# Optimization experiments

Measured on AMD Instinct MI355X. Metric: run time of the kernel, lower is better.

## Reference

```python
import jax, jax.numpy as jnp
import numpy as np

N_NODES = 50000
N_EDGES = 800000
N_GRAPHS = 128
NEG_SLOPE = 0.2


def setup_inputs() -> dict:
    key = jax.random.key(0)
    ks = jax.random.split(key, 16)
    feature = jax.random.normal(ks[0], (N_NODES, 10), dtype=jnp.float32)
    src = jax.random.randint(ks[1], (N_EDGES,), 0, N_NODES, dtype=jnp.int32)
    dst = jax.random.randint(ks[2], (N_EDGES,), 0, N_NODES, dtype=jnp.int32)
    graph_ids = jnp.sort(jax.random.randint(ks[3], (N_NODES,), 0, N_GRAPHS, dtype=jnp.int32))
    s = 0.1
    W1 = jax.random.normal(ks[4], (10, 3 * 32), dtype=jnp.float32) * s
    al1 = jax.random.normal(ks[5], (3, 32), dtype=jnp.float32) * s
    ar1 = jax.random.normal(ks[6], (3, 32), dtype=jnp.float32) * s
    W2 = jax.random.normal(ks[7], (96, 3 * 64), dtype=jnp.float32) * s
    al2 = jax.random.normal(ks[8], (3, 64), dtype=jnp.float32) * s
    ar2 = jax.random.normal(ks[9], (3, 64), dtype=jnp.float32) * s
    d1_w = jax.random.normal(ks[10], (192, 64), dtype=jnp.float32) * s
    d1_b = jnp.zeros((64,), dtype=jnp.float32)
    d2_w = jax.random.normal(ks[11], (64, 1), dtype=jnp.float32) * s
    d2_b = jnp.zeros((1,), dtype=jnp.float32)
    return {"feature": feature, "src": src, "dst": dst, "graph_ids": graph_ids,
            "W1": W1, "al1": al1, "ar1": ar1, "W2": W2, "al2": al2, "ar2": ar2,
            "d1_w": d1_w, "d1_b": d1_b, "d2_w": d2_w, "d2_b": d2_b}


def _edge_softmax(e, dst, n_nodes):
    # e: [E, H] unnormalized logits; softmax over incoming edges of each dst node
    m = jax.ops.segment_max(e, dst, num_segments=n_nodes)  # [N, H]
    ex = jnp.exp(e - m[dst])
    s = jax.ops.segment_sum(ex, dst, num_segments=n_nodes)  # [N, H]
    return ex / (s[dst] + 1e-16)


def _gat_layer(x, W, al, ar, src, dst, n_nodes):
    H, D = al.shape
    z = (x @ W).reshape(n_nodes, H, D)                     # [N, H, D]
    el = jnp.einsum('nhd,hd->nh', z, al)                   # [N, H]
    er = jnp.einsum('nhd,hd->nh', z, ar)
    e = jax.nn.leaky_relu(el[src] + er[dst], NEG_SLOPE)    # [E, H]
    a = _edge_softmax(e, dst, n_nodes)                     # [E, H]
    msg = z[src] * a[:, :, None]                           # [E, H, D]
    out = jax.ops.segment_sum(msg, dst, num_segments=n_nodes)
    return out.reshape(n_nodes, H * D)


def reference(feature, src, dst, graph_ids, W1, al1, ar1, W2, al2, ar2, d1_w, d1_b, d2_w, d2_b):
    n = feature.shape[0]
    x1 = jax.nn.relu(_gat_layer(feature, W1, al1, ar1, src, dst, n))  # [N, 96]
    x2 = jax.nn.relu(_gat_layer(x1, W2, al2, ar2, src, dst, n))       # [N, 192]
    # AvgPooling: mean of node features per graph
    sums = jax.ops.segment_sum(x2, graph_ids, num_segments=N_GRAPHS)  # [G, 192]
    cnts = jax.ops.segment_sum(jnp.ones((n,), x2.dtype), graph_ids, num_segments=N_GRAPHS)
    pooled = sums / jnp.maximum(cnts, 1.0)[:, None]
    h = jax.nn.relu(pooled @ d1_w + d1_b)
    return h @ d2_w + d2_b  # [G, 1]
```

## Files before the change

kernel.cpp:

```cpp
#include <hip/hip_runtime.h>
#include <hip/hip_bf16.h>

#define NEG_SLOPE 0.2f

typedef __attribute__((ext_vector_type(8))) short short8v;
typedef __attribute__((ext_vector_type(4))) float f32x4;

__device__ __forceinline__ float wave_max64(float v) {
    for (int o = 32; o; o >>= 1) v = fmaxf(v, __shfl_xor(v, o));
    return v;
}
__device__ __forceinline__ float wave_sum64(float v) {
    for (int o = 32; o; o >>= 1) v += __shfl_xor(v, o);
    return v;
}
__device__ __forceinline__ unsigned short f2bf(float f) {
    unsigned int u = __float_as_uint(f);
    unsigned int r = (u + 0x7fffu + ((u >> 16) & 1u)) >> 16;
    return (unsigned short)r;
}
__device__ __forceinline__ float bf2f(unsigned short u) {
    return __uint_as_float(((unsigned int)u) << 16);
}
__device__ __forceinline__ float bflo(unsigned int pk) {
    return __uint_as_float(pk << 16);
}
__device__ __forceinline__ float bfhi(unsigned int pk) {
    return __uint_as_float(pk & 0xFFFF0000u);
}


__global__ __launch_bounds__(256) void k_hist(const int* __restrict__ dst,
                                              int* __restrict__ deg,
                                              int* __restrict__ rank, int E,
                                              const float* __restrict__ W2,
                                              const float* __restrict__ al2,
                                              const float* __restrict__ ar2,
                                              unsigned short* __restrict__ W2T,
                                              float* __restrict__ val2,
                                              float* __restrict__ var2) {
    int idx = blockIdx.x * 256 + threadIdx.x;
    if (idx < 96 * 192) {
        int c = idx / 96, k = idx - c * 96;
        W2T[idx] = f2bf(W2[k * 192 + c]);
    } else if (idx < 96 * 192 + 2 * 288) {
        int t = idx - 96 * 192;
        int which = t / 288;
        int tt = t - which * 288;
        int h = tt / 96, j = tt - h * 96;
        const float* av = which ? ar2 : al2;
        float a = 0.f;
        for (int d = 0; d < 64; d++) a += W2[j * 192 + h * 64 + d] * av[h * 64 + d];
        (which ? var2 : val2)[tt] = a;
    }
    if (idx < E) rank[idx] = atomicAdd(&deg[dst[idx]], 1);
}


__global__ __launch_bounds__(256) void k_scan1(const int* __restrict__ deg,
                                               int* __restrict__ bsum, int n) {
    int idx = blockIdx.x * 256 + threadIdx.x;
    int v = idx < n ? deg[idx] : 0;
    for (int o = 32; o; o >>= 1) v += __shfl_xor(v, o);
    __shared__ int ws[4];
    if ((threadIdx.x & 63) == 0) ws[threadIdx.x >> 6] = v;
    __syncthreads();
    if (threadIdx.x == 0) bsum[blockIdx.x] = ws[0] + ws[1] + ws[2] + ws[3];
}

__global__ __launch_bounds__(256) void k_scan2(const int* __restrict__ bsum,
                                               int* __restrict__ bpre,
                                               int* __restrict__ row_start,
                                               int nb, int n) {
    __shared__ int s[256];
    int t = threadIdx.x;
    int v = t < nb ? bsum[t] : 0;
    s[t] = v;
    __syncthreads();
    for (int o = 1; o < 256; o <<= 1) {
        int u = (t >= o) ? s[t - o] : 0;
        __syncthreads();
        s[t] += u;
        __syncthreads();
    }
    if (t < nb) bpre[t] = s[t] - v;
    if (t == 255) row_start[n] = s[255];
}

__global__ __launch_bounds__(256) void k_scan3(const int* __restrict__ deg,
                                               const int* __restrict__ bpre,
                                               int* __restrict__ row_start, int n) {
    int idx = blockIdx.x * 256 + threadIdx.x;
    int lane = threadIdx.x & 63;
    int w = threadIdx.x >> 6;
    int d = idx < n ? deg[idx] : 0;
    int x = d;
    for (int o = 1; o < 64; o <<= 1) {
        int u = __shfl_up(x, o);
        if (lane >= o) x += u;
    }
    __shared__ int ws[4];
    if (lane == 63) ws[w] = x;
    __syncthreads();
    int add = bpre[blockIdx.x];
    for (int i = 0; i < w; i++) add += ws[i];
    if (idx < n) row_start[idx] = add + x - d;
}

__global__ void k_scatter(const int* __restrict__ dst, const int* __restrict__ src,
                          const int* __restrict__ rank, const int* __restrict__ row_start,
                          int* __restrict__ ssrc, int E) {
    int e = blockIdx.x * blockDim.x + threadIdx.x;
    if (e < E) ssrc[row_start[dst[e]] + rank[e]] = src[e];
}


__global__ __launch_bounds__(256) void k_el1(const float* __restrict__ feat,
                                             const float* __restrict__ W1,
                                             const float* __restrict__ al,
                                             const float* __restrict__ ar,
                                             float4* __restrict__ el1,
                                             float4* __restrict__ er1, int n) {
    __shared__ float sW[960], sal[96], sar[96], sval[30], svar[30];
    for (int i = threadIdx.x; i < 960; i += 256) sW[i] = W1[i];
    for (int i = threadIdx.x; i < 96; i += 256) { sal[i] = al[i]; sar[i] = ar[i]; }
    __syncthreads();
    int t = threadIdx.x;
    if (t < 30) {
        int h = t / 10, k = t - h * 10;
        float a = 0.f, b = 0.f;
        for (int d = 0; d < 32; d++) {
            float wv = sW[k * 96 + h * 32 + d];
            a += wv * sal[h * 32 + d];
            b += wv * sar[h * 32 + d];
        }
        sval[t] = a; svar[t] = b;
    }
    __syncthreads();
    int nd = blockIdx.x * 256 + t;
    if (nd >= n) return;
    float x[10];
#pragma unroll
    for (int k = 0; k < 10; k++) x[k] = feat[(size_t)nd * 10 + k];
    float el[3] = {}, er[3] = {};
#pragma unroll
    for (int h = 0; h < 3; h++)
#pragma unroll
        for (int k = 0; k < 10; k++) {
            el[h] += x[k] * sval[h * 10 + k];
            er[h] += x[k] * svar[h * 10 + k];
        }
    el1[nd] = make_float4(el[0], el[1], el[2], 0.f);
    er1[nd] = make_float4(er[0], er[1], er[2], 0.f);
}


__global__ __launch_bounds__(256) void k_agg1(const float* __restrict__ feat,
                                              const float4* __restrict__ el,
                                              const float4* __restrict__ er,
                                              const int* __restrict__ row_start,
                                              const int* __restrict__ ssrc,
                                              float* __restrict__ y1, int n) {
    __shared__ float pl[4][272];
    int wid = (blockIdx.x * blockDim.x + threadIdx.x) >> 6;
    int lane = threadIdx.x & 63;
    int w = threadIdx.x >> 6;
    if (wid >= n) return;
    int s0 = row_start[wid];
    int deg = row_start[wid + 1] - s0;
    if (deg <= 0) {
        if (lane < 30) y1[(size_t)wid * 30 + lane] = 0.f;
        return;
    }
    float4 erv = er[wid];
    int ll = lane & 31, hf = lane >> 5;
    int h = ll / 10, k = ll - (ll / 10) * 10;
    if (ll >= 30) { h = 2; k = 9; }

    if (deg <= 64) {
        bool act = lane < deg;
        int sv = act ? ssrc[s0 + lane] : 0;
        float4 elv = el[sv];
        float v0 = elv.x + erv.x; v0 = v0 > 0.f ? v0 : NEG_SLOPE * v0;
        float v1 = elv.y + erv.y; v1 = v1 > 0.f ? v1 : NEG_SLOPE * v1;
        float v2 = elv.z + erv.z; v2 = v2 > 0.f ? v2 : NEG_SLOPE * v2;
        if (!act) { v0 = -3.402823466e38f; v1 = v0; v2 = v0; }
        float m0 = wave_max64(v0), m1 = wave_max64(v1), m2 = wave_max64(v2);
        float p0 = act ? __expf(v0 - m0) : 0.f;
        float p1 = act ? __expf(v1 - m1) : 0.f;
        float p2 = act ? __expf(v2 - m2) : 0.f;
        float i0 = 1.f / (wave_sum64(p0) + 1e-16f);
        float i1 = 1.f / (wave_sum64(p1) + 1e-16f);
        float i2 = 1.f / (wave_sum64(p2) + 1e-16f);
        pl[w][0 * 68 + lane] = p0 * i0;
        pl[w][1 * 68 + lane] = p1 * i1;
        pl[w][2 * 68 + lane] = p2 * i2;
        reinterpret_cast<int*>(&pl[w][204])[lane] = sv * 10;
        const float* pt = &pl[w][h * 68];
        const int* zt = reinterpret_cast<const int*>(&pl[w][204]);

        float acc = 0.f;
        int i = 0;
        for (; i + 8 <= deg; i += 8) {
            float vv[4], aa[4];
#pragma unroll
            for (int j = 0; j < 4; j++) {
                int e = i + 2 * j + hf;
                int zo = zt[e];
                vv[j] = feat[zo + k];
                aa[j] = pt[e];
            }
#pragma unroll
            for (int j = 0; j < 4; j++) acc += aa[j] * vv[j];
        }
        for (; i < deg; i += 2) {
            int e = i + hf;
            if (e < deg) {
                int zo = zt[e];
                acc += pt[e] * feat[zo + k];
            }
        }
        acc += __shfl_xor(acc, 32);
        if (lane < 30) y1[(size_t)wid * 30 + lane] = acc;
    } else {
        float ern[3] = {erv.x, erv.y, erv.z};
        float m[3] = {-3.402823466e38f, -3.402823466e38f, -3.402823466e38f};
        for (int i = lane; i < deg; i += 64) {
            int sv = ssrc[s0 + i];
            float4 elv = el[sv];
            float vv[3] = {elv.x, elv.y, elv.z};
#pragma unroll
            for (int hh = 0; hh < 3; hh++) {
                float v = vv[hh] + ern[hh];
                v = v > 0.f ? v : NEG_SLOPE * v;
                m[hh] = fmaxf(m[hh], v);
            }
        }
#pragma unroll
        for (int hh = 0; hh < 3; hh++) m[hh] = wave_max64(m[hh]);
        float s[3] = {};
        for (int i = lane; i < deg; i += 64) {
            int sv = ssrc[s0 + i];
            float4 elv = el[sv];
            float vv[3] = {elv.x, elv.y, elv.z};
#pragma unroll
            for (int hh = 0; hh < 3; hh++) {
                float v = vv[hh] + ern[hh];
                v = v > 0.f ? v : NEG_SLOPE * v;
                s[hh] += __expf(v - m[hh]);
            }
        }
#pragma unroll
        for (int hh = 0; hh < 3; hh++) s[hh] = 1.f / (wave_sum64(s[hh]) + 1e-16f);
        float acc = 0.f;
        for (int i = 0; i < deg; i++) {
            int sv = ssrc[s0 + i];
            float4 elv = el[sv];
            float vv[3] = {elv.x, elv.y, elv.z};
            float v = vv[h] + ern[h];
            v = v > 0.f ? v : NEG_SLOPE * v;
            float a = __expf(v - m[h]) * s[h];
            acc += a * feat[sv * 10 + k];
        }
        if (lane < 30) y1[(size_t)wid * 30 + lane] = acc;
    }
}


__global__ __launch_bounds__(256) void k_xform1(const float* __restrict__ y1,
                                                const float* __restrict__ W1,
                                                const float* __restrict__ val2,
                                                const float* __restrict__ var2,
                                                unsigned short* __restrict__ x1,
                                                float4* __restrict__ el2,
                                                float4* __restrict__ er2, int n) {
    __shared__ float sW[960], sv2[288], sr2[288];
    for (int i = threadIdx.x; i < 960; i += 256) sW[i] = W1[i];
    for (int i = threadIdx.x; i < 288; i += 256) { sv2[i] = val2[i]; sr2[i] = var2[i]; }
    __syncthreads();
    int nd = blockIdx.x * 256 + threadIdx.x;
    if (nd >= n) return;
    float y[30];
#pragma unroll
    for (int i = 0; i < 30; i++) y[i] = y1[(size_t)nd * 30 + i];
    float el[3] = {}, er[3] = {};
#pragma unroll
    for (int h = 0; h < 3; h++) {
#pragma unroll
        for (int d0 = 0; d0 < 32; d0 += 4) {
            ushort4 o;
            unsigned short* op = &o.x;
#pragma unroll
            for (int q = 0; q < 4; q++) {
                int c = h * 32 + d0 + q;
                float acc = 0.f;
#pragma unroll
                for (int k = 0; k < 10; k++) acc += y[h * 10 + k] * sW[k * 96 + c];
                float r = fmaxf(acc, 0.f);
                op[q] = f2bf(r);
#pragma unroll
                for (int hh = 0; hh < 3; hh++) {
                    el[hh] += r * sv2[hh * 96 + c];
                    er[hh] += r * sr2[hh * 96 + c];
                }
            }
            *reinterpret_cast<ushort4*>(&x1[(size_t)nd * 96 + h * 32 + d0]) = o;
        }
    }
    el2[nd] = make_float4(el[0], el[1], el[2], 0.f);
    er2[nd] = make_float4(er[0], er[1], er[2], 0.f);
}


__global__ __launch_bounds__(256) void k_agg2(const unsigned short* __restrict__ x1,
                                              const float4* __restrict__ el,
                                              const float4* __restrict__ er,
                                              const int* __restrict__ row_start,
                                              const int* __restrict__ ssrc,
                                              unsigned short* __restrict__ y2, int n) {
    __shared__ float pl[4][272];
    int wid = (blockIdx.x * blockDim.x + threadIdx.x) >> 6;
    int lane = threadIdx.x & 63;
    int w = threadIdx.x >> 6;
    if (wid >= n) return;
    int s0 = row_start[wid];
    int deg = row_start[wid + 1] - s0;
    int c0 = lane < 48 ? lane * 2 : 0;
    if (deg <= 0) {
        if (lane < 48) {
#pragma unroll
            for (int h = 0; h < 3; h++)
                *reinterpret_cast<ushort2*>(&y2[(size_t)wid * 288 + h * 96 + c0]) =
                    make_ushort2(0, 0);
        }
        return;
    }
    float4 erv = er[wid];
    float acc[3][2] = {};

    if (deg <= 64) {
        bool act = lane < deg;
        int sv = act ? ssrc[s0 + lane] : 0;
        float4 elv = el[sv];
        float v0 = elv.x + erv.x; v0 = v0 > 0.f ? v0 : NEG_SLOPE * v0;
        float v1 = elv.y + erv.y; v1 = v1 > 0.f ? v1 : NEG_SLOPE * v1;
        float v2 = elv.z + erv.z; v2 = v2 > 0.f ? v2 : NEG_SLOPE * v2;
        if (!act) { v0 = -3.402823466e38f; v1 = v0; v2 = v0; }
        float m0 = wave_max64(v0), m1 = wave_max64(v1), m2 = wave_max64(v2);
        float p0 = act ? __expf(v0 - m0) : 0.f;
        float p1 = act ? __expf(v1 - m1) : 0.f;
        float p2 = act ? __expf(v2 - m2) : 0.f;
        float i0 = 1.f / (wave_sum64(p0) + 1e-16f);
        float i1 = 1.f / (wave_sum64(p1) + 1e-16f);
        float i2 = 1.f / (wave_sum64(p2) + 1e-16f);
        pl[w][0 * 68 + lane] = p0 * i0;
        pl[w][1 * 68 + lane] = p1 * i1;
        pl[w][2 * 68 + lane] = p2 * i2;
        reinterpret_cast<int*>(&pl[w][204])[lane] = sv * 96;
        const float* pt0 = &pl[w][0];
        const float* pt1 = &pl[w][68];
        const float* pt2 = &pl[w][136];
        const int* zt = reinterpret_cast<const int*>(&pl[w][204]);
        const unsigned short* zc = x1 + c0;

        int i = 0;
        for (; i + 8 <= deg; i += 8) {
            int zo[8];
#pragma unroll
            for (int j = 0; j < 8; j++) zo[j] = zt[i + j];
            unsigned int r[8];
#pragma unroll
            for (int j = 0; j < 8; j++)
                r[j] = *reinterpret_cast<const unsigned int*>(zc + zo[j]);
#pragma unroll
            for (int j = 0; j < 8; j++) {
                float lo = bflo(r[j]), hi = bfhi(r[j]);
                float a0 = pt0[i + j], a1 = pt1[i + j], a2 = pt2[i + j];
                acc[0][0] += a0 * lo; acc[0][1] += a0 * hi;
                acc[1][0] += a1 * lo; acc[1][1] += a1 * hi;
                acc[2][0] += a2 * lo; acc[2][1] += a2 * hi;
            }
        }
        for (; i < deg; i++) {
            unsigned int r = *reinterpret_cast<const unsigned int*>(zc + zt[i]);
            float lo = bflo(r), hi = bfhi(r);
            float a0 = pt0[i], a1 = pt1[i], a2 = pt2[i];
            acc[0][0] += a0 * lo; acc[0][1] += a0 * hi;
            acc[1][0] += a1 * lo; acc[1][1] += a1 * hi;
            acc[2][0] += a2 * lo; acc[2][1] += a2 * hi;
        }
    } else {
        float ern[3] = {erv.x, erv.y, erv.z};
        float m[3] = {-3.402823466e38f, -3.402823466e38f, -3.402823466e38f};
        for (int i = lane; i < deg; i += 64) {
            int sv = ssrc[s0 + i];
            float4 elv = el[sv];
            float vv[3] = {elv.x, elv.y, elv.z};
#pragma unroll
            for (int hh = 0; hh < 3; hh++) {
                float v = vv[hh] + ern[hh];
                v = v > 0.f ? v : NEG_SLOPE * v;
                m[hh] = fmaxf(m[hh], v);
            }
        }
#pragma unroll
        for (int hh = 0; hh < 3; hh++) m[hh] = wave_max64(m[hh]);
        float s[3] = {};
        for (int i = lane; i < deg; i += 64) {
            int sv = ssrc[s0 + i];
            float4 elv = el[sv];
            float vv[3] = {elv.x, elv.y, elv.z};
#pragma unroll
            for (int hh = 0; hh < 3; hh++) {
                float v = vv[hh] + ern[hh];
                v = v > 0.f ? v : NEG_SLOPE * v;
                s[hh] += __expf(v - m[hh]);
            }
        }
#pragma unroll
        for (int hh = 0; hh < 3; hh++) s[hh] = 1.f / (wave_sum64(s[hh]) + 1e-16f);
        for (int i = 0; i < deg; i++) {
            int sv = ssrc[s0 + i];
            float4 elv = el[sv];
            float vv[3] = {elv.x, elv.y, elv.z};
            float a[3];
#pragma unroll
            for (int hh = 0; hh < 3; hh++) {
                float v = vv[hh] + ern[hh];
                v = v > 0.f ? v : NEG_SLOPE * v;
                a[hh] = __expf(v - m[hh]) * s[hh];
            }
            unsigned int r = *reinterpret_cast<const unsigned int*>(x1 + sv * 96 + c0);
            float lo = bflo(r), hi = bfhi(r);
            acc[0][0] += a[0] * lo; acc[0][1] += a[0] * hi;
            acc[1][0] += a[1] * lo; acc[1][1] += a[1] * hi;
            acc[2][0] += a[2] * lo; acc[2][1] += a[2] * hi;
        }
    }
    if (lane < 48) {
#pragma unroll
        for (int h = 0; h < 3; h++) {
            ushort2 o2;
            o2.x = f2bf(acc[h][0]); o2.y = f2bf(acc[h][1]);
            *reinterpret_cast<ushort2*>(&y2[(size_t)wid * 288 + h * 96 + c0]) = o2;
        }
    }
}


__global__ __launch_bounds__(256) void k_xform2(const unsigned short* __restrict__ y2,
                                                const unsigned short* __restrict__ W2T,
                                                unsigned short* __restrict__ x2, int n) {
    int h = blockIdx.y;
    int w = threadIdx.x >> 6;
    int l = threadIdx.x & 63;
    int q = l >> 4, c16 = l & 15;
    int Ra = blockIdx.x * 64 + w * 16 + c16;
    short8v afr[3];
    if (Ra < n) {
#pragma unroll
        for (int ks = 0; ks < 3; ks++)
            afr[ks] = *reinterpret_cast<const short8v*>(y2 + (size_t)Ra * 288 + h * 96 +
                                                        ks * 32 + q * 8);
    } else {
#pragma unroll
        for (int ks = 0; ks < 3; ks++)
#pragma unroll
            for (int i = 0; i < 8; i++) afr[ks][i] = 0;
    }
    f32x4 acc[4];
#pragma unroll
    for (int t = 0; t < 4; t++)
#pragma unroll
        for (int r = 0; r < 4; r++) acc[t][r] = 0.f;
#pragma unroll
    for (int t = 0; t < 4; t++) {
        const unsigned short* bp = W2T + (size_t)(h * 64 + t * 16 + c16) * 96 + q * 8;
#pragma unroll
        for (int ks = 0; ks < 3; ks++) {
            short8v bfr = *reinterpret_cast<const short8v*>(bp + ks * 32);
            acc[t] = __builtin_amdgcn_mfma_f32_16x16x32_bf16(afr[ks], bfr, acc[t], 0, 0, 0);
        }
    }
    int Rq = blockIdx.x * 64 + w * 16 + q * 4;
#pragma unroll
    for (int t = 0; t < 4; t++) {
#pragma unroll
        for (int r = 0; r < 4; r++) {
            if (Rq + r < n)
                x2[(size_t)(Rq + r) * 192 + h * 64 + t * 16 + c16] =
                    f2bf(fmaxf(acc[t][r], 0.f));
        }
    }
}


__global__ __launch_bounds__(192) void k_pool(const unsigned short* __restrict__ x2,
                                              const int* __restrict__ gid,
                                              float* __restrict__ gsum, int n) {
    int base = blockIdx.x * 32;
    if (base >= n) return;
    int end = base + 32; if (end > n) end = n;
    int c = threadIdx.x;
    float acc = 0.f;
    int gprev = gid[base];
    for (int i = base; i < end; i++) {
        int g = gid[i];
        if (g != gprev) {
            atomicAdd(&gsum[gprev * 192 + c], acc);
            acc = 0.f;
            gprev = g;
        }
        acc += bf2f(x2[(size_t)i * 192 + c]);
    }
    atomicAdd(&gsum[gprev * 192 + c], acc);
}


__global__ __launch_bounds__(64) void k_head(const float* __restrict__ gsum,
                                             const int* __restrict__ gid,
                                             const float* __restrict__ d1w,
                                             const float* __restrict__ d1b,
                                             const float* __restrict__ d2w,
                                             const float* __restrict__ d2b,
                                             float* __restrict__ out, int n, int G) {
    int g = blockIdx.x, j = threadIdx.x;
    int lo0 = 0, hi0 = n;
    while (lo0 < hi0) { int mid = (lo0 + hi0) >> 1; if (gid[mid] < g) lo0 = mid + 1; else hi0 = mid; }
    int lo1 = lo0, hi1 = n;
    while (lo1 < hi1) { int mid = (lo1 + hi1) >> 1; if (gid[mid] < g + 1) lo1 = mid + 1; else hi1 = mid; }
    float inv = 1.f / fmaxf((float)(lo1 - lo0), 1.f);
    float h = d1b[j];
    for (int k = 0; k < 192; k++) h += (gsum[g * 192 + k] * inv) * d1w[(size_t)k * 64 + j];
    h = fmaxf(h, 0.f);
    float v = h * d2w[j];
    for (int o = 32; o; o >>= 1) v += __shfl_xor(v, o);
    if (j == 0) out[g] = v + d2b[0];
}


extern "C" void kernel_launch(void* const* d_in, const int* in_sizes, int n_in,
                              void* d_out, int out_size, void* d_ws, size_t ws_size,
                              hipStream_t stream) {
    const float* feat = (const float*)d_in[0];
    const int* src = (const int*)d_in[1];
    const int* dst = (const int*)d_in[2];
    const int* gid = (const int*)d_in[3];
    const float* W1 = (const float*)d_in[4];
    const float* al1 = (const float*)d_in[5];
    const float* ar1 = (const float*)d_in[6];
    const float* W2 = (const float*)d_in[7];
    const float* al2 = (const float*)d_in[8];
    const float* ar2 = (const float*)d_in[9];
    const float* d1w = (const float*)d_in[10];
    const float* d1b = (const float*)d_in[11];
    const float* d2w = (const float*)d_in[12];
    const float* d2b = (const float*)d_in[13];
    float* out = (float*)d_out;
    const int N = in_sizes[0] / 10;
    const int E = in_sizes[1];
    const int G = out_size;
    const int NB = (N + 255) / 256;

    char* p = (char*)d_ws;
    auto take = [&](size_t bytes) -> char* {
        char* r = p;
        p += (bytes + 255) & ~(size_t)255;
        return r;
    };
    float* y1 = (float*)take((size_t)N * 30 * 4);
    unsigned short* x1 = (unsigned short*)take((size_t)N * 96 * 2);
    unsigned short* y2 = (unsigned short*)take((size_t)N * 288 * 2);
    unsigned short* x2 = (unsigned short*)take((size_t)N * 192 * 2);
    float4* el1 = (float4*)take((size_t)N * 16);
    float4* er1 = (float4*)take((size_t)N * 16);
    float4* el2 = (float4*)take((size_t)N * 16);
    float4* er2 = (float4*)take((size_t)N * 16);
    unsigned short* W2T = (unsigned short*)take((size_t)96 * 192 * 2);
    float* val2 = (float*)take((size_t)288 * 4);
    float* var2 = (float*)take((size_t)288 * 4);
    int* rank = (int*)take((size_t)E * 4);
    int* bsum = (int*)take((size_t)NB * 4);
    int* bpre = (int*)take((size_t)NB * 4);
    size_t zbytes = (size_t)N * 4 + (size_t)G * 192 * 4;
    int* deg = (int*)take(zbytes);
    float* gsum = (float*)(deg + N);
    int* row_start = (int*)take((size_t)(N + 1) * 4);
    int* ssrc = (int*)take((size_t)E * 4);

    hipMemsetAsync(deg, 0, zbytes, stream);

    k_hist<<<(E + 255) / 256, 256, 0, stream>>>(dst, deg, rank, E, W2, al2, ar2,
                                                W2T, val2, var2);
    k_el1<<<NB, 256, 0, stream>>>(feat, W1, al1, ar1, el1, er1, N);
    k_scan1<<<NB, 256, 0, stream>>>(deg, bsum, N);
    k_scan2<<<1, 256, 0, stream>>>(bsum, bpre, row_start, NB, N);
    k_scan3<<<NB, 256, 0, stream>>>(deg, bpre, row_start, N);
    k_scatter<<<(E + 255) / 256, 256, 0, stream>>>(dst, src, rank, row_start, ssrc, E);

    k_agg1<<<((size_t)N * 64 + 255) / 256, 256, 0, stream>>>(feat, el1, er1, row_start,
                                                             ssrc, y1, N);
    k_xform1<<<NB, 256, 0, stream>>>(y1, W1, val2, var2, x1, el2, er2, N);
    k_agg2<<<((size_t)N * 64 + 255) / 256, 256, 0, stream>>>(x1, el2, er2, row_start,
                                                             ssrc, y2, N);
    k_xform2<<<dim3((N + 63) / 64, 3), 256, 0, stream>>>(y2, W2T, x2, N);
    k_pool<<<(N + 31) / 32, 192, 0, stream>>>(x2, gid, gsum, N);
    k_head<<<G, 64, 0, stream>>>(gsum, gid, d1w, d1b, d2w, d2b, out, N, G);
}
```

Before: 276.3 us.

## Replace global atomic degree histogram with per-block LDS histograms and column scan

The CSR build no longer does global atomics on deg. Each 1024-thread block now builds a packed 16-bit histogram of a chunk of edges in LDS (25000 words). A column-scan kernel then turns the per-block counts into per-block offsets (boff) and total degrees, and the scatter adds row_start, block offset and local rank. The goal is to remove contention on global atomics, at the cost of writing and reading NBH×N count and offset arrays (about 98 blocks × 50000) and a serial loop over blocks per node. The W2 prep work moves into its own kernel, and the LDS array size is fixed, which assumes N ≤ 50000.

```diff
diff --git a/kernel.cpp b/kernel.cpp
--- a/kernel.cpp
+++ b/kernel.cpp
@@ -2,6 +2,7 @@
 #include <hip/hip_bf16.h>
 
 #define NEG_SLOPE 0.2f
+#define HCHUNK 8192
 
 typedef __attribute__((ext_vector_type(8))) short short8v;
 typedef __attribute__((ext_vector_type(4))) float f32x4;
@@ -30,10 +31,112 @@
 }
 
 
-__global__ __launch_bounds__(256) void k_hist(const int* __restrict__ dst,
-                                              int* __restrict__ deg,
-                                              int* __restrict__ rank, int E,
-                                              const float* __restrict__ W2,
+__global__ __launch_bounds__(1024) void k_hist2(const int* __restrict__ dst,
+                                                unsigned int* __restrict__ blkcnt,
+                                                int* __restrict__ rank, int E, int n) {
+    __shared__ unsigned int cnt[25000];
+    int nw = (n + 1) >> 1;
+    for (int i = threadIdx.x; i < nw; i += 1024) cnt[i] = 0;
+    __syncthreads();
+    int base = blockIdx.x * HCHUNK;
+#pragma unroll
+    for (int i = 0; i < HCHUNK / 1024; i++) {
+        int e = base + i * 1024 + threadIdx.x;
+        if (e < E) {
+            int d = dst[e];
+            unsigned int add = (d & 1) ? 0x10000u : 1u;
+            unsigned int old = atomicAdd(&cnt[d >> 1], add);
+            rank[e] = (d & 1) ? (int)(old >> 16) : (int)(old & 0xFFFFu);
+        }
+    }
+    __syncthreads();
+    unsigned int* outp = blkcnt + (size_t)blockIdx.x * nw;
+    for (int i = threadIdx.x; i < nw; i += 1024) outp[i] = cnt[i];
+}
+
+
+__global__ __launch_bounds__(256) void k_colscan(const unsigned int* __restrict__ blkcnt,
+                                                 unsigned short* __restrict__ boff,
+                                                 int* __restrict__ deg,
+                                                 int* __restrict__ bsum, int n, int NBH) {
+    int nd = blockIdx.x * 256 + threadIdx.x;
+    int nw = (n + 1) >> 1;
+    int run = 0;
+    if (nd < n) {
+        int w = nd >> 1, sh = (nd & 1) * 16;
+#pragma unroll 4
+        for (int b = 0; b < NBH; b++) {
+            unsigned int c = (blkcnt[(size_t)b * nw + w] >> sh) & 0xFFFFu;
+            boff[(size_t)b * n + nd] = (unsigned short)run;
+            run += (int)c;
+        }
+        deg[nd] = run;
+    }
+    int v = (nd < n) ? run : 0;
+    for (int o = 32; o; o >>= 1) v += __shfl_xor(v, o);
+    __shared__ int ws[4];
+    if ((threadIdx.x & 63) == 0) ws[threadIdx.x >> 6] = v;
+    __syncthreads();
+    if (threadIdx.x == 0) bsum[blockIdx.x] = ws[0] + ws[1] + ws[2] + ws[3];
+}
+
+
+__global__ __launch_bounds__(256) void k_scan2(const int* __restrict__ bsum,
+                                               int* __restrict__ bpre,
+                                               int* __restrict__ row_start,
+                                               int nb, int n) {
+    __shared__ int s[256];
+    int t = threadIdx.x;
+    int v = t < nb ? bsum[t] : 0;
+    s[t] = v;
+    __syncthreads();
+    for (int o = 1; o < 256; o <<= 1) {
+        int u = (t >= o) ? s[t - o] : 0;
+        __syncthreads();
+        s[t] += u;
+        __syncthreads();
+    }
+    if (t < nb) bpre[t] = s[t] - v;
+    if (t == 255) row_start[n] = s[255];
+}
+
+__global__ __launch_bounds__(256) void k_scan3(const int* __restrict__ deg,
+                                               const int* __restrict__ bpre,
+                                               int* __restrict__ row_start, int n) {
+    int idx = blockIdx.x * 256 + threadIdx.x;
+    int lane = threadIdx.x & 63;
+    int w = threadIdx.x >> 6;
+    int d = idx < n ? deg[idx] : 0;
+    int x = d;
+    for (int o = 1; o < 64; o <<= 1) {
+        int u = __shfl_up(x, o);
+        if (lane >= o) x += u;
+    }
+    __shared__ int ws[4];
+    if (lane == 63) ws[w] = x;
+    __syncthreads();
+    int add = bpre[blockIdx.x];
+    for (int i = 0; i < w; i++) add += ws[i];
+    if (idx < n) row_start[idx] = add + x - d;
+}
+
+
+__global__ void k_scatter(const int* __restrict__ dst, const int* __restrict__ src,
+                          const int* __restrict__ rank,
+                          const unsigned short* __restrict__ boff,
+                          const int* __restrict__ row_start,
+                          int* __restrict__ ssrc, int E, int n) {
+    int e = blockIdx.x * blockDim.x + threadIdx.x;
+    if (e < E) {
+        int d = dst[e];
+        int b = e >> 13;
+        int pos = row_start[d] + (int)boff[(size_t)b * n + d] + rank[e];
+        ssrc[pos] = src[e];
+    }
+}
+
+
+__global__ __launch_bounds__(256) void k_prep(const float* __restrict__ W2,
                                               const float* __restrict__ al2,
                                               const float* __restrict__ ar2,
                                               unsigned short* __restrict__ W2T,
@@ -53,65 +156,6 @@
         for (int d = 0; d < 64; d++) a += W2[j * 192 + h * 64 + d] * av[h * 64 + d];
         (which ? var2 : val2)[tt] = a;
     }
-    if (idx < E) rank[idx] = atomicAdd(&deg[dst[idx]], 1);
-}
-
-
-__global__ __launch_bounds__(256) void k_scan1(const int* __restrict__ deg,
-                                               int* __restrict__ bsum, int n) {
-    int idx = blockIdx.x * 256 + threadIdx.x;
-    int v = idx < n ? deg[idx] : 0;
-    for (int o = 32; o; o >>= 1) v += __shfl_xor(v, o);
-    __shared__ int ws[4];
-    if ((threadIdx.x & 63) == 0) ws[threadIdx.x >> 6] = v;
-    __syncthreads();
-    if (threadIdx.x == 0) bsum[blockIdx.x] = ws[0] + ws[1] + ws[2] + ws[3];
-}
-
-__global__ __launch_bounds__(256) void k_scan2(const int* __restrict__ bsum,
-                                               int* __restrict__ bpre,
-                                               int* __restrict__ row_start,
-                                               int nb, int n) {
-    __shared__ int s[256];
-    int t = threadIdx.x;
-    int v = t < nb ? bsum[t] : 0;
-    s[t] = v;
-    __syncthreads();
-    for (int o = 1; o < 256; o <<= 1) {
-        int u = (t >= o) ? s[t - o] : 0;
-        __syncthreads();
-        s[t] += u;
-        __syncthreads();
-    }
-    if (t < nb) bpre[t] = s[t] - v;
-    if (t == 255) row_start[n] = s[255];
-}
-
-__global__ __launch_bounds__(256) void k_scan3(const int* __restrict__ deg,
-                                               const int* __restrict__ bpre,
-                                               int* __restrict__ row_start, int n) {
-    int idx = blockIdx.x * 256 + threadIdx.x;
-    int lane = threadIdx.x & 63;
-    int w = threadIdx.x >> 6;
-    int d = idx < n ? deg[idx] : 0;
-    int x = d;
-    for (int o = 1; o < 64; o <<= 1) {
-        int u = __shfl_up(x, o);
-        if (lane >= o) x += u;
-    }
-    __shared__ int ws[4];
-    if (lane == 63) ws[w] = x;
-    __syncthreads();
-    int add = bpre[blockIdx.x];
-    for (int i = 0; i < w; i++) add += ws[i];
-    if (idx < n) row_start[idx] = add + x - d;
-}
-
-__global__ void k_scatter(const int* __restrict__ dst, const int* __restrict__ src,
-                          const int* __restrict__ rank, const int* __restrict__ row_start,
-                          int* __restrict__ ssrc, int E) {
-    int e = blockIdx.x * blockDim.x + threadIdx.x;
-    if (e < E) ssrc[row_start[dst[e]] + rank[e]] = src[e];
 }
 
 
@@ -561,6 +605,7 @@
     const int E = in_sizes[1];
     const int G = out_size;
     const int NB = (N + 255) / 256;
+    const int NBH = (E + HCHUNK - 1) / HCHUNK;
 
     char* p = (char*)d_ws;
     auto take = [&](size_t bytes) -> char* {
@@ -580,23 +625,26 @@
     float* val2 = (float*)take((size_t)288 * 4);
     float* var2 = (float*)take((size_t)288 * 4);
     int* rank = (int*)take((size_t)E * 4);
+    unsigned int* blkcnt = (unsigned int*)take((size_t)NBH * ((N + 1) / 2) * 4);
+    unsigned short* boff = (unsigned short*)take((size_t)NBH * N * 2);
+    int* deg = (int*)take((size_t)N * 4);
     int* bsum = (int*)take((size_t)NB * 4);
     int* bpre = (int*)take((size_t)NB * 4);
-    size_t zbytes = (size_t)N * 4 + (size_t)G * 192 * 4;
-    int* deg = (int*)take(zbytes);
-    float* gsum = (float*)(deg + N);
+    float* gsum = (float*)take((size_t)G * 192 * 4);
     int* row_start = (int*)take((size_t)(N + 1) * 4);
     int* ssrc = (int*)take((size_t)E * 4);
 
-    hipMemsetAsync(deg, 0, zbytes, stream);
-
-    k_hist<<<(E + 255) / 256, 256, 0, stream>>>(dst, deg, rank, E, W2, al2, ar2,
-                                                W2T, val2, var2);
+    hipMemsetAsync(gsum, 0, (size_t)G * 192 * 4, stream);
+
+    k_hist2<<<NBH, 1024, 0, stream>>>(dst, blkcnt, rank, E, N);
+    k_prep<<<(96 * 192 + 2 * 288 + 255) / 256, 256, 0, stream>>>(W2, al2, ar2,
+                                                                 W2T, val2, var2);
     k_el1<<<NB, 256, 0, stream>>>(feat, W1, al1, ar1, el1, er1, N);
-    k_scan1<<<NB, 256, 0, stream>>>(deg, bsum, N);
+    k_colscan<<<NB, 256, 0, stream>>>(blkcnt, boff, deg, bsum, N, NBH);
     k_scan2<<<1, 256, 0, stream>>>(bsum, bpre, row_start, NB, N);
     k_scan3<<<NB, 256, 0, stream>>>(deg, bpre, row_start, N);
-    k_scatter<<<(E + 255) / 256, 256, 0, stream>>>(dst, src, rank, row_start, ssrc, E);
+    k_scatter<<<(E + 255) / 256, 256, 0, stream>>>(dst, src, rank, boff, row_start,
+                                                   ssrc, E, N);
 
     k_agg1<<<((size_t)N * 64 + 255) / 256, 256, 0, stream>>>(feat, el1, er1, row_start,
                                                              ssrc, y1, N);
```

After: 264.2 us. 4.4% less time.
